# Optimization experiments

Hardware: AMD Instinct MI355X
Metric: run time of the kernel (lower is better)

Reference implementation:

```python
import jax, jax.numpy as jnp
import numpy as np

RF = 16       # receptive_field
STRIDE = 16   # sim_strides
ALPHA = 0.3   # tf.keras LeakyReLU default alpha
EPS = 1e-3    # tf.keras BatchNormalization default epsilon


def _leaky(x):
    return jnp.where(x > 0, x, ALPHA * x)


def _bn_train(x, gamma, beta):
    # training-mode batch norm over (B, H, W), channel-last
    mu = jnp.mean(x, axis=(0, 1, 2))
    var = jnp.var(x, axis=(0, 1, 2))
    return (x - mu) * jax.lax.rsqrt(var + EPS) * gamma + beta


def _cbl(x, W, gamma, beta):
    # 1x1 conv (== channel matmul) + BN + LeakyReLU
    y = jnp.einsum('bhwc,cd->bhwd', x, W)
    return _leaky(_bn_train(y, gamma, beta))


def setup_inputs() -> dict:
    key = jax.random.key(0)
    ks = jax.random.split(key, 4)
    B, H, Wd, C = 4, 64, 64, 256
    s = 1.0 / np.sqrt(C)
    return {
        'inputs': jax.random.normal(ks[0], (B, H, Wd, C), jnp.float32),
        'Wq': jax.random.normal(ks[1], (C, C), jnp.float32) * s,
        'gq': jnp.ones((C,), jnp.float32), 'bq': jnp.zeros((C,), jnp.float32),
        'Wk': jax.random.normal(ks[2], (C, C), jnp.float32) * s,
        'gk': jnp.ones((C,), jnp.float32), 'bk': jnp.zeros((C,), jnp.float32),
        'Wv': jax.random.normal(ks[3], (C, C), jnp.float32) * s,
        'gv': jnp.ones((C,), jnp.float32), 'bv': jnp.zeros((C,), jnp.float32),
        'g1': jnp.ones((C,), jnp.float32), 'b1': jnp.zeros((C,), jnp.float32),
    }


def _windows(x):
    # x: [B,H,W,C] -> [B, nH*nW, RF, RF, C] overlapping-capable window gather
    H, Wd = x.shape[1], x.shape[2]
    nH = (H - RF) // STRIDE + 1
    nW = (Wd - RF) // STRIDE + 1
    ih = (jnp.arange(nH) * STRIDE)[:, None] + jnp.arange(RF)[None, :]  # [nH,RF]
    iw = (jnp.arange(nW) * STRIDE)[:, None] + jnp.arange(RF)[None, :]  # [nW,RF]
    xw = x[:, ih][:, :, :, iw]            # [B,nH,RF,nW,RF,C]
    xw = xw.transpose(0, 1, 3, 2, 4, 5)   # [B,nH,nW,RF,RF,C]
    return xw.reshape(x.shape[0], nH * nW, RF, RF, x.shape[3])


def reference(inputs, Wq, gq, bq, Wk, gk, bk, Wv, gv, bv, g1, b1):
    Q = _cbl(inputs, Wq, gq, bq)   # [B,H,W,C]
    K = _cbl(inputs, Wk, gk, bk)
    V = _cbl(inputs, Wv, gv, bv)
    C = Q.shape[-1]
    Kw = _windows(K)               # [B,N,RF,RF,C]
    Vw = _windows(V)
    # full-Q x window-K attention, summed over windows (matches nested loop)
    scores = jnp.einsum('bijc,bnpqc->bnijpq', Q, Kw) / jnp.sqrt(jnp.asarray(C, Q.dtype))
    scores = _leaky(scores)
    yout = jnp.einsum('bnijpq,bnpqc->bijc', scores, Vw)  # sum over windows n
    y = _bn_train(yout, g1, b1)
    # softmax jointly over spatial axes (1,2)
    m = jnp.max(y, axis=(1, 2), keepdims=True)
    e = jnp.exp(y - m)
    return e / jnp.sum(e, axis=(1, 2), keepdims=True)
```

## Files before the change

kernel.cpp:

```cpp
#include <hip/hip_runtime.h>
#include <stdint.h>


typedef __attribute__((ext_vector_type(8)))  short short8;
typedef __attribute__((ext_vector_type(4)))  float f32x4;
typedef __attribute__((ext_vector_type(16))) float f32x16;
typedef __attribute__((ext_vector_type(4)))  unsigned short ushort4v;

#define ALPHA 0.3f
#define EPS   1e-3
#define NTOT  16384.0

__device__ __forceinline__ unsigned short f2bf(float f){
  unsigned u = __float_as_uint(f);
  u += 0x7FFFu + ((u>>16)&1u);
  return (unsigned short)(u>>16);
}
__device__ __forceinline__ float lrelu(float x){ return fmaxf(x, ALPHA*x); }

__global__ __launch_bounds__(256)
void k_prep(const float* __restrict__ X,
            const float* __restrict__ Wq,
            const float* __restrict__ Wk,
            const float* __restrict__ Wv,
            unsigned short* __restrict__ Xb,
            unsigned short* __restrict__ Wt,
            float* __restrict__ zws){
  int blk = blockIdx.x, tid = threadIdx.x;
  if (blk < 4096){
    int i = (blk*256 + tid)*4;
    float4 v = *(const float4*)(X + i);
    ushort4v o; o.x = f2bf(v.x); o.y = f2bf(v.y); o.z = f2bf(v.z); o.w = f2bf(v.w);
    *(ushort4v*)(Xb + i) = o;
  } else {
    int o = (blk - 4096)*256 + tid;
    int p = o >> 16, rem = o & 65535;
    int j = rem >> 8, c = rem & 255;
    const float* W = (p==0) ? Wq : ((p==1) ? Wk : Wv);
    Wt[o] = f2bf(W[c*256 + j]);
    if (o < 5120) zws[o] = 0.f;
  }
}

__global__ __launch_bounds__(256)
void k_qkv_gemm(const unsigned short* __restrict__ X,
                const unsigned short* __restrict__ Wt,
                float* __restrict__ YQK, float* __restrict__ Yv,
                double* __restrict__ st){
  __shared__ __align__(16) unsigned short At[64*264];
  __shared__ __align__(16) unsigned short Bt[64*264];
  int tid = threadIdx.x;
  int mb = blockIdx.x, nb = blockIdx.y;
#pragma unroll
  for (int it = 0; it < 8; ++it){
    int s = it*256 + tid;
    int row = s >> 5, ch = s & 31;
    uint4 a = *(const uint4*)(X  + ((size_t)(mb*64 + row))*256 + ch*8);
    uint4 b = *(const uint4*)(Wt + ((size_t)(nb*64 + row))*256 + ch*8);
    *(uint4*)(At + row*264 + ch*8) = a;
    *(uint4*)(Bt + row*264 + ch*8) = b;
  }
  __syncthreads();
  int lane = tid & 63, wv = tid >> 6;
  int ln15 = lane & 15, quad = lane >> 4;
  int rw = (wv & 1)*32, cw = (wv >> 1)*32;
  f32x4 acc[2][2] = {};
#pragma unroll
  for (int ks = 0; ks < 8; ++ks){
    short8 afr[2], bfr[2];
#pragma unroll
    for (int mt = 0; mt < 2; ++mt){
      int r = rw + mt*16 + ln15;
      afr[mt] = *(const short8*)(At + r*264 + (ks*4+quad)*8);
    }
#pragma unroll
    for (int nt = 0; nt < 2; ++nt){
      int r = cw + nt*16 + ln15;
      bfr[nt] = *(const short8*)(Bt + r*264 + (ks*4+quad)*8);
    }
#pragma unroll
    for (int mt = 0; mt < 2; ++mt)
#pragma unroll
      for (int nt = 0; nt < 2; ++nt)
        acc[mt][nt] = __builtin_amdgcn_mfma_f32_16x16x32_bf16(afr[mt], bfr[nt], acc[mt][nt], 0,0,0);
  }
  float ps[2] = {0.f, 0.f}, pq[2] = {0.f, 0.f};
#pragma unroll
  for (int mt = 0; mt < 2; ++mt)
#pragma unroll
    for (int nt = 0; nt < 2; ++nt)
#pragma unroll
      for (int r = 0; r < 4; ++r){
        float v = acc[mt][nt][r];
        ps[nt] += v; pq[nt] += v*v;
      }
  if (nb < 8){
    int proj = nb >> 2;
    float* base = YQK + (size_t)proj*(16384*256);
    int l5c = ln15 >> 3, j = ln15 & 7;
#pragma unroll
    for (int mt = 0; mt < 2; ++mt){
      int g = (mb*64 + rw + mt*16) >> 5;
      int l31r0 = ((rw + mt*16) & 31) + quad*4;
#pragma unroll
      for (int nt = 0; nt < 2; ++nt){
        int ks2 = ((nb & 3)*64 + cw + nt*16) >> 4;
#pragma unroll
        for (int r = 0; r < 4; ++r){
          size_t chunk = (size_t)((g*16 + ks2)*64 + l5c*32 + l31r0 + r);
          base[chunk*8 + j] = acc[mt][nt][r];
        }
      }
    }
  } else {
    int vc0 = (nb - 8)*64 + cw;
#pragma unroll
    for (int mt = 0; mt < 2; ++mt)
#pragma unroll
      for (int nt = 0; nt < 2; ++nt)
#pragma unroll
        for (int r = 0; r < 4; ++r){
          int row = mb*64 + rw + mt*16 + quad*4 + r;
          Yv[(size_t)row*256 + vc0 + nt*16 + ln15] = acc[mt][nt][r];
        }
  }
  __syncthreads();
  float* red = (float*)At;
  if (tid < 128) red[tid] = 0.f;
  __syncthreads();
#pragma unroll
  for (int nt = 0; nt < 2; ++nt){
    int colL = cw + nt*16 + ln15;
    atomicAdd(&red[colL],      ps[nt]);
    atomicAdd(&red[64 + colL], pq[nt]);
  }
  __syncthreads();
  if (tid < 64){
    int cc = nb*64 + tid;
    atomicAdd(&st[cc],       (double)red[tid]);
    atomicAdd(&st[768 + cc], (double)red[64 + tid]);
  }
}

__global__ __launch_bounds__(256)
void k_bn(const float* __restrict__ YQK, const float* __restrict__ Yv,
          const double* __restrict__ st,
          const float* __restrict__ gq, const float* __restrict__ bq,
          const float* __restrict__ gk, const float* __restrict__ bk,
          const float* __restrict__ gv, const float* __restrict__ bv,
          unsigned short* __restrict__ Qf, unsigned short* __restrict__ Kf,
          unsigned short* __restrict__ Vf){
  __shared__ float sc_s[256], sh_s[256];
  __shared__ unsigned short tile[64][66];
  int tid = threadIdx.x;
  int blk = blockIdx.x;
  if (blk < 4096){
    int proj = blk >> 11;
    {
      int c = tid;
      int cc = proj*256 + c;
      double mu  = st[cc]     * (1.0/NTOT);
      double var = st[768+cc] * (1.0/NTOT) - mu*mu;
      double g = proj ? (double)gk[c] : (double)gq[c];
      double b = proj ? (double)bk[c] : (double)bq[c];
      double a = g / sqrt(var + EPS);
      float f = proj ? 1.f : 0.0625f;
      sc_s[c] = (float)a * f;
      sh_s[c] = (float)(b - mu*a) * f;
    }
    __syncthreads();
    int oc = blk*256 + tid;
    int rest = oc & 524287;
    int ks = (rest >> 6) & 15, l5c = (rest >> 5) & 1;
    int ch0 = ks*16 + l5c*8;
    const float* src = YQK + (size_t)oc*8;
    float4 v0 = *(const float4*)(src);
    float4 v1 = *(const float4*)(src + 4);
    const float* sc = sc_s + ch0;
    const float* sh = sh_s + ch0;
    unsigned short r[8];
    r[0]=f2bf(lrelu(v0.x*sc[0]+sh[0])); r[1]=f2bf(lrelu(v0.y*sc[1]+sh[1]));
    r[2]=f2bf(lrelu(v0.z*sc[2]+sh[2])); r[3]=f2bf(lrelu(v0.w*sc[3]+sh[3]));
    r[4]=f2bf(lrelu(v1.x*sc[4]+sh[4])); r[5]=f2bf(lrelu(v1.y*sc[5]+sh[5]));
    r[6]=f2bf(lrelu(v1.z*sc[6]+sh[6])); r[7]=f2bf(lrelu(v1.w*sc[7]+sh[7]));
    uint4 u;
    u.x = (unsigned)r[0] | ((unsigned)r[1]<<16);
    u.y = (unsigned)r[2] | ((unsigned)r[3]<<16);
    u.z = (unsigned)r[4] | ((unsigned)r[5]<<16);
    u.w = (unsigned)r[6] | ((unsigned)r[7]<<16);
    *(uint4*)((proj ? Kf : Qf) + (size_t)rest*8) = u;
  } else {
    int b2 = blk - 4096;
    int pt = b2 & 63, ct = (b2 >> 6) & 3, b = b2 >> 8;
    if (tid < 64){
      int c = ct*64 + tid;
      int cc = 512 + c;
      double mu  = st[cc]     * (1.0/NTOT);
      double var = st[768+cc] * (1.0/NTOT) - mu*mu;
      double a = (double)gv[c] / sqrt(var + EPS);
      sc_s[tid] = (float)a;
      sh_s[tid] = (float)((double)bv[c] - mu*a);
    }
    __syncthreads();
    int cl = tid & 63, rq = tid >> 6;
    int c  = ct*64 + cl;
    float sc = sc_s[cl], sh = sh_s[cl];
#pragma unroll 4
    for (int k = 0; k < 16; ++k){
      int r = k*4 + rq;
      size_t t = (size_t)b*4096 + pt*64 + r;
      float v = Yv[t*256 + c];
      tile[r][cl] = f2bf(lrelu(v*sc + sh));
    }
    __syncthreads();
#pragma unroll
    for (int it = 0; it < 2; ++it){
      int m = it*256 + tid;
      int c2 = m >> 3, kg = m & 7;
      int ch = ct*64 + c2;
      int gc = b*8 + (ch >> 5), l31c = ch & 31;
      int kp = pt*4 + (kg >> 1), l5k = kg & 1;
      unsigned short r0 = tile[kg*8+0][c2], r1 = tile[kg*8+1][c2];
      unsigned short r2 = tile[kg*8+2][c2], r3 = tile[kg*8+3][c2];
      unsigned short r4 = tile[kg*8+4][c2], r5 = tile[kg*8+5][c2];
      unsigned short r6 = tile[kg*8+6][c2], r7 = tile[kg*8+7][c2];
      uint4 u;
      u.x = (unsigned)r0 | ((unsigned)r1<<16);
      u.y = (unsigned)r2 | ((unsigned)r3<<16);
      u.z = (unsigned)r4 | ((unsigned)r5<<16);
      u.w = (unsigned)r6 | ((unsigned)r7<<16);
      *(uint4*)(Vf + ((size_t)((gc*256 + kp)*64 + l5k*32 + l31c))*8) = u;
    }
  }
}

__global__ __launch_bounds__(512, 4)
void k_attn(const unsigned short* __restrict__ Qf,
            const unsigned short* __restrict__ Kf,
            const unsigned short* __restrict__ Vf,
            float* __restrict__ P0, float* __restrict__ P1){
  __shared__ __align__(16) unsigned short Ql[64*256];
  __shared__ __align__(16) unsigned short Sl[64*264];
  int tid = threadIdx.x;
  int blk = blockIdx.x;
  int qt = blk >> 3, combo = blk & 7;
  int b = combo >> 1, half = combo & 1;
  int q0 = qt*64;
  int lane = tid & 63, w = tid >> 6;
  int l31 = lane & 31, l5 = lane >> 5;
  float* P = half ? P1 : P0;

  int gq0 = b*128 + qt*2;
  {
    const uint4* src = (const uint4*)(Qf + (size_t)gq0*8192);
    uint4* dst = (uint4*)Ql;
#pragma unroll
    for (int it = 0; it < 4; ++it) dst[it*512 + tid] = src[it*512 + tid];
  }
  __syncthreads();

  f32x16 acc2[2] = {};
  int gk0 = b*128 + half*64 + w;
  const unsigned short* kb = Kf + (size_t)gk0*8192 + lane*8;
  const unsigned short* vb = Vf + ((size_t)((b*8 + w)*256 + half*128))*512 + lane*8;
  const unsigned short* qa0 = Ql + lane*8;
  const unsigned short* qa1 = Ql + 16*512 + lane*8;

  for (int kt = 0; kt < 8; ++kt){
    f32x16 a1[2] = {};
    const unsigned short* kbt = kb + (size_t)kt*8*8192;
    __builtin_amdgcn_s_setprio(1);
#pragma unroll
    for (int ks = 0; ks < 16; ++ks){
      short8 kf = *(const short8*)(kbt + ks*512);
      short8 q0v = *(const short8*)(qa0 + ks*512);
      short8 q1v = *(const short8*)(qa1 + ks*512);
      a1[0] = __builtin_amdgcn_mfma_f32_32x32x16_bf16(q0v, kf, a1[0], 0, 0, 0);
      a1[1] = __builtin_amdgcn_mfma_f32_32x32x16_bf16(q1v, kf, a1[1], 0, 0, 0);
    }
    __builtin_amdgcn_s_setprio(0);
    __syncthreads();
#pragma unroll
    for (int reg = 0; reg < 16; ++reg){
      int rloc = (reg & 3) + 8*(reg >> 2) + 4*l5;
      float x0 = a1[0][reg], x1 = a1[1][reg];
      Sl[rloc*264 + w*32 + l31]        = f2bf(fmaxf(x0, 0.3f*x0));
      Sl[(32 + rloc)*264 + w*32 + l31] = f2bf(fmaxf(x1, 0.3f*x1));
    }
    __syncthreads();
    const unsigned short* vbt = vb + (size_t)kt*16*512;
    __builtin_amdgcn_s_setprio(1);
#pragma unroll
    for (int kk = 0; kk < 16; ++kk){
      short8 vf = *(const short8*)(vbt + kk*512);
      short8 s0 = *(const short8*)(Sl + (     l31)*264 + kk*16 + l5*8);
      short8 s1 = *(const short8*)(Sl + (32 + l31)*264 + kk*16 + l5*8);
      acc2[0] = __builtin_amdgcn_mfma_f32_32x32x16_bf16(s0, vf, acc2[0], 0, 0, 0);
      acc2[1] = __builtin_amdgcn_mfma_f32_32x32x16_bf16(s1, vf, acc2[1], 0, 0, 0);
    }
    __builtin_amdgcn_s_setprio(0);
  }
#pragma unroll
  for (int c = 0; c < 2; ++c)
#pragma unroll
    for (int reg = 0; reg < 16; ++reg){
      int row = q0 + c*32 + (reg & 3) + 8*(reg >> 2) + 4*l5;
      P[((size_t)b*4096 + row)*256 + w*32 + l31] = acc2[c][reg];
    }
}

__global__ __launch_bounds__(256)
void k_red(const float* __restrict__ P0, const float* __restrict__ P1,
           float* __restrict__ yout, double* __restrict__ st){
  int tid = threadIdx.x;
  int r0 = blockIdx.x*32;
  double sum = 0, sq = 0;
#pragma unroll 4
  for (int r = 0; r < 32; ++r){
    size_t idx = (size_t)(r0 + r)*256 + tid;
    float v = P0[idx] + P1[idx];
    yout[idx] = v;
    sum += v; sq += (double)v*v;
  }
  atomicAdd(&st[1536 + tid], sum);
  atomicAdd(&st[1792 + tid], sq);
}

__global__ __launch_bounds__(256)
void k_soft1(const float* __restrict__ yout, const double* __restrict__ st,
             const float* __restrict__ g1, float* __restrict__ sums){
  __shared__ float red[256];
  __shared__ float sA[64], sK[64];
  int tid = threadIdx.x;
  int chunk = blockIdx.x, ct = blockIdx.y, b = blockIdx.z;
  int cl = tid & 63, pg = tid >> 6;
  int c = ct*64 + cl;
  if (tid < 64){
    int cc = ct*64 + tid;
    double mu  = st[1536 + cc]*(1.0/NTOT);
    double var = st[1792 + cc]*(1.0/NTOT) - mu*mu;
    double a = g1[cc] / sqrt(var + EPS);
    sA[tid] = (float)a;
    sK[tid] = (float)(a*mu);
  }
  __syncthreads();
  float a = sA[cl], K = sK[cl];
  float s = 0.f;
  const float* base = yout + ((size_t)b*4096 + chunk*256)*256 + c;
#pragma unroll 4
  for (int k = 0; k < 64; ++k){
    float v = base[(size_t)(pg + k*4)*256];
    s += __expf(v*a - K);
  }
  red[tid] = s;
  __syncthreads();
  if (tid < 64){
    float tot = red[tid] + red[64+tid] + red[128+tid] + red[192+tid];
    atomicAdd(&sums[b*256 + ct*64 + tid], tot);
  }
}

__global__ __launch_bounds__(256)
void k_soft2(const float* __restrict__ yout, const double* __restrict__ st,
             const float* __restrict__ g1, const float* __restrict__ sums,
             float* __restrict__ out){
  __shared__ float sA[64], sK[64], sR[64];
  int tid = threadIdx.x;
  int chunk = blockIdx.x, ct = blockIdx.y, b = blockIdx.z;
  int cl = tid & 63, pg = tid >> 6;
  int c = ct*64 + cl;
  if (tid < 64){
    int cc = ct*64 + tid;
    double mu  = st[1536 + cc]*(1.0/NTOT);
    double var = st[1792 + cc]*(1.0/NTOT) - mu*mu;
    double a = g1[cc] / sqrt(var + EPS);
    sA[tid] = (float)a;
    sK[tid] = (float)(a*mu);
    sR[tid] = 1.f / sums[b*256 + cc];
  }
  __syncthreads();
  float a = sA[cl], K = sK[cl], rl = sR[cl];
  const float* base = yout + ((size_t)b*4096 + chunk*256)*256 + c;
  float* obase = out + ((size_t)b*4096 + chunk*256)*256 + c;
#pragma unroll 4
  for (int k = 0; k < 64; ++k){
    size_t idx = (size_t)(pg + k*4)*256;
    obase[idx] = __expf(base[idx]*a - K) * rl;
  }
}

extern "C" void kernel_launch(void* const* d_in, const int* in_sizes, int n_in,
                              void* d_out, int out_size, void* d_ws, size_t ws_size,
                              hipStream_t stream){
  (void)in_sizes; (void)n_in; (void)out_size; (void)ws_size;
  const float* X  = (const float*)d_in[0];
  const float* Wq = (const float*)d_in[1];
  const float* gq = (const float*)d_in[2];
  const float* bq = (const float*)d_in[3];
  const float* Wk = (const float*)d_in[4];
  const float* gk = (const float*)d_in[5];
  const float* bk = (const float*)d_in[6];
  const float* Wv = (const float*)d_in[7];
  const float* gv = (const float*)d_in[8];
  const float* bv = (const float*)d_in[9];
  const float* g1 = (const float*)d_in[10];

  char* ws = (char*)d_ws;
  double*         st   = (double*)ws;
  float*          sums = (float*)(ws + 16384);
  unsigned short* Wt   = (unsigned short*)(ws + 26624);
  unsigned short* Xb   = (unsigned short*)(ws + 419840);
  float*          YQK  = (float*)(ws + 8808448);
  float*          Yv   = (float*)(ws + 42362880);
  unsigned short* Kf   = (unsigned short*)(ws + 59140096);
  unsigned short* Vf   = (unsigned short*)(ws + 67528704);
  unsigned short* Qf   = Xb;
  float*          P0   = YQK;
  float*          P1   = (float*)((char*)YQK + 16777216);
  float*          yo   = Yv;

  k_prep    <<<4864, 256, 0, stream>>>(X, Wq, Wk, Wv, Xb, Wt, (float*)st);
  k_qkv_gemm<<<dim3(256,12), 256, 0, stream>>>(Xb, Wt, YQK, Yv, st);
  k_bn      <<<5120, 256, 0, stream>>>(YQK, Yv, st, gq, bq, gk, bk, gv, bv, Qf, Kf, Vf);
  k_attn    <<<512, 512, 0, stream>>>(Qf, Kf, Vf, P0, P1);
  k_red     <<<512, 256, 0, stream>>>(P0, P1, yo, st);
  k_soft1   <<<dim3(16,4,4), 256, 0, stream>>>(yo, st, g1, sums);
  k_soft2   <<<dim3(16,4,4), 256, 0, stream>>>(yo, st, g1, sums, (float*)d_out);
}
```

Measured before the change: 251.2 us.

## Derive QKV batch-norm stats from input Gram matrix and fuse BN into GEMM

Instead of writing fp32 Q/K/V projections to memory, reducing their statistics, and running a separate BN pass, the code computes the input Gram matrix X^T X and per-channel input sums. From these it derives each projection channel's mean and variance as w^T G w and w·xsum. The QKV GEMM then applies BN scale/shift and LeakyReLU in its epilogue and writes bf16 in the attention layout directly. This removes large fp32 intermediate traffic and a kernel, but adds a Gram kernel with float atomics. It also computes variance as E[y²]−mu² in float from bf16 inputs, which may lose accuracy.

Measured after the change: 273.1 us. 1.09x slower.

```diff
diff --git a/kernel.cpp b/kernel.cpp
--- a/kernel.cpp
+++ b/kernel.cpp
@@ -16,7 +16,9 @@
   u += 0x7FFFu + ((u>>16)&1u);
   return (unsigned short)(u>>16);
 }
-__device__ __forceinline__ float lrelu(float x){ return fmaxf(x, ALPHA*x); }
+__device__ __forceinline__ float bf2f(unsigned short u){
+  return __uint_as_float((unsigned)u << 16);
+}
 
 __global__ __launch_bounds__(256)
 void k_prep(const float* __restrict__ X,
@@ -25,7 +27,7 @@
             const float* __restrict__ Wv,
             unsigned short* __restrict__ Xb,
             unsigned short* __restrict__ Wt,
-            float* __restrict__ zws){
+            float* __restrict__ Gz, float* __restrict__ stz){
   int blk = blockIdx.x, tid = threadIdx.x;
   if (blk < 4096){
     int i = (blk*256 + tid)*4;
@@ -33,24 +35,142 @@
     ushort4v o; o.x = f2bf(v.x); o.y = f2bf(v.y); o.z = f2bf(v.z); o.w = f2bf(v.w);
     *(ushort4v*)(Xb + i) = o;
   } else {
-    int o = (blk - 4096)*256 + tid;
+    int zb = blk - 4096;
+    int o = zb*256 + tid;
     int p = o >> 16, rem = o & 65535;
     int j = rem >> 8, c = rem & 255;
     const float* W = (p==0) ? Wq : ((p==1) ? Wk : Wv);
     Wt[o] = f2bf(W[c*256 + j]);
-    if (o < 5120) zws[o] = 0.f;
+    if (zb < 257)            Gz[o] = 0.f;
+    else if (zb < 265)       stz[(zb-257)*256 + tid] = 0.f;
+  }
+}
+
+__global__ __launch_bounds__(256)
+void k_gram(const unsigned short* __restrict__ Xb,
+            float* __restrict__ G, float* __restrict__ xsum){
+  __shared__ __align__(16) unsigned short At[64*72];
+  __shared__ __align__(16) unsigned short Bt[64*72];
+  int tid = threadIdx.x;
+  int ci = blockIdx.x, cj = blockIdx.y, ks = blockIdx.z;
+  bool diag = (ci == cj);
+  int lane = tid & 63, wv = tid >> 6;
+  int ln15 = lane & 15, quad = lane >> 4;
+  int rw = (wv & 1)*32, cw = (wv >> 1)*32;
+  f32x4 acc[2][2] = {};
+  float xs = 0.f;
+  int r0 = ks*1024;
+  int trl = tid >> 3, c8 = tid & 7;
+  for (int s = 0; s < 16; ++s){
+    int rbase = r0 + s*64;
+#pragma unroll
+    for (int i2 = 0; i2 < 2; ++i2){
+      int t = i2*32 + trl;
+      uint4 a = *(const uint4*)(Xb + ((size_t)(rbase + t))*256 + ci*64 + c8*8);
+      const unsigned short* ap = (const unsigned short*)&a;
+#pragma unroll
+      for (int e = 0; e < 8; ++e) At[(c8*8+e)*72 + t] = ap[e];
+      if (!diag){
+        uint4 b = *(const uint4*)(Xb + ((size_t)(rbase + t))*256 + cj*64 + c8*8);
+        const unsigned short* bp = (const unsigned short*)&b;
+#pragma unroll
+        for (int e = 0; e < 8; ++e) Bt[(c8*8+e)*72 + t] = bp[e];
+      }
+    }
+    __syncthreads();
+    if (diag && tid < 64){
+      float s2 = 0.f;
+      for (int t = 0; t < 64; ++t) s2 += bf2f(At[tid*72 + t]);
+      xs += s2;
+    }
+    const unsigned short* Bu = diag ? At : Bt;
+#pragma unroll
+    for (int k0 = 0; k0 < 2; ++k0){
+      short8 af[2], bf[2];
+#pragma unroll
+      for (int mt = 0; mt < 2; ++mt)
+        af[mt] = *(const short8*)(At + (rw+mt*16+ln15)*72 + k0*32 + quad*8);
+#pragma unroll
+      for (int nt = 0; nt < 2; ++nt)
+        bf[nt] = *(const short8*)(Bu + (cw+nt*16+ln15)*72 + k0*32 + quad*8);
+#pragma unroll
+      for (int mt = 0; mt < 2; ++mt)
+#pragma unroll
+        for (int nt = 0; nt < 2; ++nt)
+          acc[mt][nt] = __builtin_amdgcn_mfma_f32_16x16x32_bf16(af[mt], bf[nt], acc[mt][nt], 0,0,0);
+    }
+    __syncthreads();
+  }
+#pragma unroll
+  for (int mt = 0; mt < 2; ++mt)
+#pragma unroll
+    for (int nt = 0; nt < 2; ++nt)
+#pragma unroll
+      for (int r = 0; r < 4; ++r){
+        int gr = ci*64 + rw + mt*16 + quad*4 + r;
+        int gc = cj*64 + cw + nt*16 + ln15;
+        atomicAdd(&G[gr*256 + gc], acc[mt][nt][r]);
+      }
+  if (diag && tid < 64) atomicAdd(&xsum[ci*64 + tid], xs);
+}
+
+__global__ __launch_bounds__(256)
+void k_coef2(const float* __restrict__ G, const float* __restrict__ xsum,
+             const unsigned short* __restrict__ Wt,
+             const float* __restrict__ gq, const float* __restrict__ bq,
+             const float* __restrict__ gk, const float* __restrict__ bk,
+             const float* __restrict__ gv, const float* __restrict__ bv,
+             float* __restrict__ scv, float* __restrict__ shv){
+  __shared__ float wv_s[256];
+  __shared__ float red1[256], red2[256];
+  int n = blockIdx.x;
+  int c = threadIdx.x;
+  float w = bf2f(Wt[n*256 + c]);
+  wv_s[c] = w;
+  __syncthreads();
+  const float* gr = G + c*256;
+  float dot = 0.f;
+#pragma unroll 8
+  for (int c2 = 0; c2 < 256; c2 += 4){
+    float4 g4 = *(const float4*)(gr + c2);
+    dot += g4.x*wv_s[c2] + g4.y*wv_s[c2+1] + g4.z*wv_s[c2+2] + g4.w*wv_s[c2+3];
+  }
+  red1[c] = w * dot;
+  red2[c] = xsum[c] * w;
+  __syncthreads();
+  for (int off = 128; off > 0; off >>= 1){
+    if (c < off){ red1[c] += red1[c+off]; red2[c] += red2[c+off]; }
+    __syncthreads();
+  }
+  if (c == 0){
+    double ms = (double)red1[0] * (1.0/NTOT);
+    double mu = (double)red2[0] * (1.0/NTOT);
+    double var = ms - mu*mu;
+    int proj = n >> 8, ch = n & 255;
+    double g = (proj==0) ? gq[ch] : (proj==1) ? gk[ch] : gv[ch];
+    double b = (proj==0) ? bq[ch] : (proj==1) ? bk[ch] : bv[ch];
+    double a = g / sqrt(var + EPS);
+    double f = (proj==0) ? 0.0625 : 1.0;
+    scv[n] = (float)(a*f);
+    shv[n] = (float)((b - mu*a)*f);
   }
 }
 
 __global__ __launch_bounds__(256)
 void k_qkv_gemm(const unsigned short* __restrict__ X,
                 const unsigned short* __restrict__ Wt,
-                float* __restrict__ YQK, float* __restrict__ Yv,
-                double* __restrict__ st){
+                const float* __restrict__ scv, const float* __restrict__ shv,
+                unsigned short* __restrict__ Qf, unsigned short* __restrict__ Kf,
+                unsigned short* __restrict__ Vf){
   __shared__ __align__(16) unsigned short At[64*264];
   __shared__ __align__(16) unsigned short Bt[64*264];
+  __shared__ float cf_sc[64], cf_sh[64];
   int tid = threadIdx.x;
   int mb = blockIdx.x, nb = blockIdx.y;
+  if (tid < 64){
+    int idx = (nb < 8) ? ((nb>>2)*256 + (nb&3)*64 + tid) : (512 + (nb-8)*64 + tid);
+    cf_sc[tid] = scv[idx]; cf_sh[tid] = shv[idx];
+  }
 #pragma unroll
   for (int it = 0; it < 8; ++it){
     int s = it*256 + tid;
@@ -84,151 +204,57 @@
       for (int nt = 0; nt < 2; ++nt)
         acc[mt][nt] = __builtin_amdgcn_mfma_f32_16x16x32_bf16(afr[mt], bfr[nt], acc[mt][nt], 0,0,0);
   }
-  float ps[2] = {0.f, 0.f}, pq[2] = {0.f, 0.f};
+  float scr[2], shr[2];
+#pragma unroll
+  for (int nt = 0; nt < 2; ++nt){
+    int cl = cw + nt*16 + ln15;
+    scr[nt] = cf_sc[cl]; shr[nt] = cf_sh[cl];
+  }
+  __syncthreads();
+  unsigned short* tile = (unsigned short*)At;
 #pragma unroll
   for (int mt = 0; mt < 2; ++mt)
 #pragma unroll
     for (int nt = 0; nt < 2; ++nt)
 #pragma unroll
       for (int r = 0; r < 4; ++r){
-        float v = acc[mt][nt][r];
-        ps[nt] += v; pq[nt] += v*v;
+        int row = rw + mt*16 + quad*4 + r;
+        int col = cw + nt*16 + ln15;
+        float v = acc[mt][nt][r]*scr[nt] + shr[nt];
+        tile[row*72 + col] = f2bf(fmaxf(v, ALPHA*v));
       }
+  __syncthreads();
   if (nb < 8){
-    int proj = nb >> 2;
-    float* base = YQK + (size_t)proj*(16384*256);
-    int l5c = ln15 >> 3, j = ln15 & 7;
-#pragma unroll
-    for (int mt = 0; mt < 2; ++mt){
-      int g = (mb*64 + rw + mt*16) >> 5;
-      int l31r0 = ((rw + mt*16) & 31) + quad*4;
-#pragma unroll
-      for (int nt = 0; nt < 2; ++nt){
-        int ks2 = ((nb & 3)*64 + cw + nt*16) >> 4;
-#pragma unroll
-        for (int r = 0; r < 4; ++r){
-          size_t chunk = (size_t)((g*16 + ks2)*64 + l5c*32 + l31r0 + r);
-          base[chunk*8 + j] = acc[mt][nt][r];
-        }
-      }
-    }
-  } else {
-    int vc0 = (nb - 8)*64 + cw;
-#pragma unroll
-    for (int mt = 0; mt < 2; ++mt)
-#pragma unroll
-      for (int nt = 0; nt < 2; ++nt)
-#pragma unroll
-        for (int r = 0; r < 4; ++r){
-          int row = mb*64 + rw + mt*16 + quad*4 + r;
-          Yv[(size_t)row*256 + vc0 + nt*16 + ln15] = acc[mt][nt][r];
-        }
-  }
-  __syncthreads();
-  float* red = (float*)At;
-  if (tid < 128) red[tid] = 0.f;
-  __syncthreads();
-#pragma unroll
-  for (int nt = 0; nt < 2; ++nt){
-    int colL = cw + nt*16 + ln15;
-    atomicAdd(&red[colL],      ps[nt]);
-    atomicAdd(&red[64 + colL], pq[nt]);
-  }
-  __syncthreads();
-  if (tid < 64){
-    int cc = nb*64 + tid;
-    atomicAdd(&st[cc],       (double)red[tid]);
-    atomicAdd(&st[768 + cc], (double)red[64 + tid]);
-  }
-}
-
-__global__ __launch_bounds__(256)
-void k_bn(const float* __restrict__ YQK, const float* __restrict__ Yv,
-          const double* __restrict__ st,
-          const float* __restrict__ gq, const float* __restrict__ bq,
-          const float* __restrict__ gk, const float* __restrict__ bk,
-          const float* __restrict__ gv, const float* __restrict__ bv,
-          unsigned short* __restrict__ Qf, unsigned short* __restrict__ Kf,
-          unsigned short* __restrict__ Vf){
-  __shared__ float sc_s[256], sh_s[256];
-  __shared__ unsigned short tile[64][66];
-  int tid = threadIdx.x;
-  int blk = blockIdx.x;
-  if (blk < 4096){
-    int proj = blk >> 11;
-    {
-      int c = tid;
-      int cc = proj*256 + c;
-      double mu  = st[cc]     * (1.0/NTOT);
-      double var = st[768+cc] * (1.0/NTOT) - mu*mu;
-      double g = proj ? (double)gk[c] : (double)gq[c];
-      double b = proj ? (double)bk[c] : (double)bq[c];
-      double a = g / sqrt(var + EPS);
-      float f = proj ? 1.f : 0.0625f;
-      sc_s[c] = (float)a * f;
-      sh_s[c] = (float)(b - mu*a) * f;
-    }
-    __syncthreads();
-    int oc = blk*256 + tid;
-    int rest = oc & 524287;
-    int ks = (rest >> 6) & 15, l5c = (rest >> 5) & 1;
-    int ch0 = ks*16 + l5c*8;
-    const float* src = YQK + (size_t)oc*8;
-    float4 v0 = *(const float4*)(src);
-    float4 v1 = *(const float4*)(src + 4);
-    const float* sc = sc_s + ch0;
-    const float* sh = sh_s + ch0;
-    unsigned short r[8];
-    r[0]=f2bf(lrelu(v0.x*sc[0]+sh[0])); r[1]=f2bf(lrelu(v0.y*sc[1]+sh[1]));
-    r[2]=f2bf(lrelu(v0.z*sc[2]+sh[2])); r[3]=f2bf(lrelu(v0.w*sc[3]+sh[3]));
-    r[4]=f2bf(lrelu(v1.x*sc[4]+sh[4])); r[5]=f2bf(lrelu(v1.y*sc[5]+sh[5]));
-    r[6]=f2bf(lrelu(v1.z*sc[6]+sh[6])); r[7]=f2bf(lrelu(v1.w*sc[7]+sh[7]));
-    uint4 u;
-    u.x = (unsigned)r[0] | ((unsigned)r[1]<<16);
-    u.y = (unsigned)r[2] | ((unsigned)r[3]<<16);
-    u.z = (unsigned)r[4] | ((unsigned)r[5]<<16);
-    u.w = (unsigned)r[6] | ((unsigned)r[7]<<16);
-    *(uint4*)((proj ? Kf : Qf) + (size_t)rest*8) = u;
-  } else {
-    int b2 = blk - 4096;
-    int pt = b2 & 63, ct = (b2 >> 6) & 3, b = b2 >> 8;
-    if (tid < 64){
-      int c = ct*64 + tid;
-      int cc = 512 + c;
-      double mu  = st[cc]     * (1.0/NTOT);
-      double var = st[768+cc] * (1.0/NTOT) - mu*mu;
-      double a = (double)gv[c] / sqrt(var + EPS);
-      sc_s[tid] = (float)a;
-      sh_s[tid] = (float)((double)bv[c] - mu*a);
-    }
-    __syncthreads();
-    int cl = tid & 63, rq = tid >> 6;
-    int c  = ct*64 + cl;
-    float sc = sc_s[cl], sh = sh_s[cl];
-#pragma unroll 4
-    for (int k = 0; k < 16; ++k){
-      int r = k*4 + rq;
-      size_t t = (size_t)b*4096 + pt*64 + r;
-      float v = Yv[t*256 + c];
-      tile[r][cl] = f2bf(lrelu(v*sc + sh));
-    }
-    __syncthreads();
+    unsigned short* dstB = (nb >> 2) ? Kf : Qf;
 #pragma unroll
     for (int it = 0; it < 2; ++it){
       int m = it*256 + tid;
-      int c2 = m >> 3, kg = m & 7;
-      int ch = ct*64 + c2;
-      int gc = b*8 + (ch >> 5), l31c = ch & 31;
-      int kp = pt*4 + (kg >> 1), l5k = kg & 1;
-      unsigned short r0 = tile[kg*8+0][c2], r1 = tile[kg*8+1][c2];
-      unsigned short r2 = tile[kg*8+2][c2], r3 = tile[kg*8+3][c2];
-      unsigned short r4 = tile[kg*8+4][c2], r5 = tile[kg*8+5][c2];
-      unsigned short r6 = tile[kg*8+6][c2], r7 = tile[kg*8+7][c2];
+      int cg = m >> 6, row = m & 63;
+      uint4 u = *(const uint4*)(tile + row*72 + cg*8);
+      int ch_g = (nb&3)*64 + cg*8;
+      int ksf = ch_g >> 4, l5c = (ch_g >> 3) & 1;
+      int row_g = mb*64 + row;
+      int g = row_g >> 5, l31r = row_g & 31;
+      *(uint4*)(dstB + ((size_t)((g*16 + ksf)*64 + l5c*32 + l31r))*8) = u;
+    }
+  } else {
+    int b = mb >> 6;
+#pragma unroll
+    for (int it = 0; it < 2; ++it){
+      int m = it*256 + tid;
+      int chl = m & 63, pg = m >> 6;
+      unsigned short r0 = tile[(pg*8+0)*72 + chl], r1 = tile[(pg*8+1)*72 + chl];
+      unsigned short r2 = tile[(pg*8+2)*72 + chl], r3 = tile[(pg*8+3)*72 + chl];
+      unsigned short r4 = tile[(pg*8+4)*72 + chl], r5 = tile[(pg*8+5)*72 + chl];
+      unsigned short r6 = tile[(pg*8+6)*72 + chl], r7 = tile[(pg*8+7)*72 + chl];
       uint4 u;
       u.x = (unsigned)r0 | ((unsigned)r1<<16);
       u.y = (unsigned)r2 | ((unsigned)r3<<16);
       u.z = (unsigned)r4 | ((unsigned)r5<<16);
       u.w = (unsigned)r6 | ((unsigned)r7<<16);
+      int ch_g = (nb-8)*64 + chl;
+      int gc = b*8 + (ch_g >> 5), l31c = ch_g & 31;
+      int kp = (mb&63)*4 + (pg >> 1), l5k = pg & 1;
       *(uint4*)(Vf + ((size_t)((gc*256 + kp)*64 + l5k*32 + l31c))*8) = u;
     }
   }
@@ -310,7 +336,7 @@
 }
 
 __global__ __launch_bounds__(256)
-void k_red(const float* __restrict__ P0, const float* __restrict__ P1,
+void k_red(const float* __restrict__ P0c, const float* __restrict__ P1,
            float* __restrict__ yout, double* __restrict__ st){
   int tid = threadIdx.x;
   int r0 = blockIdx.x*32;
@@ -318,7 +344,7 @@
 #pragma unroll 4
   for (int r = 0; r < 32; ++r){
     size_t idx = (size_t)(r0 + r)*256 + tid;
-    float v = P0[idx] + P1[idx];
+    float v = P0c[idx] + P1[idx];
     yout[idx] = v;
     sum += v; sq += (double)v*v;
   }
@@ -407,21 +433,25 @@
 
   char* ws = (char*)d_ws;
   double*         st   = (double*)ws;
+  float*          stz  = (float*)(ws + 12288);
   float*          sums = (float*)(ws + 16384);
+  float*          scv  = (float*)(ws + 20480);
+  float*          shv  = (float*)(ws + 23552);
   unsigned short* Wt   = (unsigned short*)(ws + 26624);
   unsigned short* Xb   = (unsigned short*)(ws + 419840);
-  float*          YQK  = (float*)(ws + 8808448);
-  float*          Yv   = (float*)(ws + 42362880);
-  unsigned short* Kf   = (unsigned short*)(ws + 59140096);
-  unsigned short* Vf   = (unsigned short*)(ws + 67528704);
-  unsigned short* Qf   = Xb;
-  float*          P0   = YQK;
-  float*          P1   = (float*)((char*)YQK + 16777216);
-  float*          yo   = Yv;
-
-  k_prep    <<<4864, 256, 0, stream>>>(X, Wq, Wk, Wv, Xb, Wt, (float*)st);
-  k_qkv_gemm<<<dim3(256,12), 256, 0, stream>>>(Xb, Wt, YQK, Yv, st);
-  k_bn      <<<5120, 256, 0, stream>>>(YQK, Yv, st, gq, bq, gk, bk, gv, bv, Qf, Kf, Vf);
+  float*          G    = (float*)(ws + 8808448);
+  float*          xsum = (float*)(ws + 9070592);
+  unsigned short* Qf   = (unsigned short*)(ws + 17301504);
+  unsigned short* Kf   = (unsigned short*)(ws + 25690112);
+  unsigned short* Vf   = (unsigned short*)(ws + 34078720);
+  float*          P0   = (float*)(ws + 419840);
+  float*          P1   = (float*)(ws + 42467328);
+  float*          yo   = P0;
+
+  k_prep    <<<4864, 256, 0, stream>>>(X, Wq, Wk, Wv, Xb, Wt, G, stz);
+  k_gram    <<<dim3(4,4,16), 256, 0, stream>>>(Xb, G, xsum);
+  k_coef2   <<<768, 256, 0, stream>>>(G, xsum, Wt, gq, bq, gk, bk, gv, bv, scv, shv);
+  k_qkv_gemm<<<dim3(256,12), 256, 0, stream>>>(Xb, Wt, scv, shv, Qf, Kf, Vf);
   k_attn    <<<512, 512, 0, stream>>>(Qf, Kf, Vf, P0, P1);
   k_red     <<<512, 256, 0, stream>>>(P0, P1, yo, st);
   k_soft1   <<<dim3(16,4,4), 256, 0, stream>>>(yo, st, g1, sums);
```

## Fuse split-K reduction into attention epilogue and merge softmax passes cooperatively

Applied to the files above, without the earlier changes.

The attention kernel now has the second-finishing block of each half pair, detected with an atomic counter, add the partner's partial sum, write the combined result and accumulate the batch-norm statistics. This removes the separate reduction kernel and one full read/write pass over the partials. The two softmax kernels become one cooperative kernel that keeps the exponentials in registers across a grid-wide sync, so the activations are read once instead of twice. In exchange it adds a threadfence/atomic handshake, a large per-thread register array, and a dependency on cooperative launch residency.

Measured after the change: 458.8 us. 82.6% more time.

```diff
diff --git a/kernel.cpp b/kernel.cpp
--- a/kernel.cpp
+++ b/kernel.cpp
@@ -1,5 +1,8 @@
 #include <hip/hip_runtime.h>
+#include <hip/hip_cooperative_groups.h>
 #include <stdint.h>
+
+namespace cg = cooperative_groups;
 
 
 typedef __attribute__((ext_vector_type(8)))  short short8;
@@ -38,7 +41,7 @@
     int j = rem >> 8, c = rem & 255;
     const float* W = (p==0) ? Wq : ((p==1) ? Wk : Wv);
     Wt[o] = f2bf(W[c*256 + j]);
-    if (o < 5120) zws[o] = 0.f;
+    if (o < 5376) zws[o] = 0.f;
   }
 }
 
@@ -238,7 +241,8 @@
 void k_attn(const unsigned short* __restrict__ Qf,
             const unsigned short* __restrict__ Kf,
             const unsigned short* __restrict__ Vf,
-            float* __restrict__ P0, float* __restrict__ P1){
+            float* __restrict__ P0, float* __restrict__ P1,
+            unsigned* __restrict__ cnt, double* __restrict__ st){
   __shared__ __align__(16) unsigned short Ql[64*256];
   __shared__ __align__(16) unsigned short Sl[64*264];
   int tid = threadIdx.x;
@@ -307,63 +311,40 @@
       int row = q0 + c*32 + (reg & 3) + 8*(reg >> 2) + 4*l5;
       P[((size_t)b*4096 + row)*256 + w*32 + l31] = acc2[c][reg];
     }
+  __threadfence();
+  __shared__ unsigned sOld;
+  __syncthreads();
+  if (tid == 0) sOld = atomicAdd(&cnt[(b<<6) + qt], 1u);
+  __syncthreads();
+  if (sOld == 0) return;
+  __threadfence();
+  const float* Po = half ? P0 : P1;
+  double sum = 0.0, sq = 0.0;
+#pragma unroll
+  for (int c = 0; c < 2; ++c)
+#pragma unroll
+    for (int reg = 0; reg < 16; ++reg){
+      int row = q0 + c*32 + (reg & 3) + 8*(reg >> 2) + 4*l5;
+      size_t idx = ((size_t)b*4096 + row)*256 + w*32 + l31;
+      float v = acc2[c][reg] + Po[idx];
+      P0[idx] = v;
+      sum += v; sq += (double)v*v;
+    }
+  double* redS = (double*)Sl;
+  redS[tid] = sum; redS[512 + tid] = sq;
+  __syncthreads();
+  if ((tid & 32) == 0){
+    int c = ((tid >> 6) << 5) + (tid & 31);
+    atomicAdd(&st[1536 + c], redS[tid] + redS[tid + 32]);
+    atomicAdd(&st[1792 + c], redS[512 + tid] + redS[512 + tid + 32]);
+  }
 }
 
 __global__ __launch_bounds__(256)
-void k_red(const float* __restrict__ P0, const float* __restrict__ P1,
-           float* __restrict__ yout, double* __restrict__ st){
-  int tid = threadIdx.x;
-  int r0 = blockIdx.x*32;
-  double sum = 0, sq = 0;
-#pragma unroll 4
-  for (int r = 0; r < 32; ++r){
-    size_t idx = (size_t)(r0 + r)*256 + tid;
-    float v = P0[idx] + P1[idx];
-    yout[idx] = v;
-    sum += v; sq += (double)v*v;
-  }
-  atomicAdd(&st[1536 + tid], sum);
-  atomicAdd(&st[1792 + tid], sq);
-}
-
-__global__ __launch_bounds__(256)
-void k_soft1(const float* __restrict__ yout, const double* __restrict__ st,
-             const float* __restrict__ g1, float* __restrict__ sums){
+void k_soft(const float* __restrict__ yout, const double* __restrict__ st,
+            const float* __restrict__ g1, float* __restrict__ sums,
+            float* __restrict__ out){
   __shared__ float red[256];
-  __shared__ float sA[64], sK[64];
-  int tid = threadIdx.x;
-  int chunk = blockIdx.x, ct = blockIdx.y, b = blockIdx.z;
-  int cl = tid & 63, pg = tid >> 6;
-  int c = ct*64 + cl;
-  if (tid < 64){
-    int cc = ct*64 + tid;
-    double mu  = st[1536 + cc]*(1.0/NTOT);
-    double var = st[1792 + cc]*(1.0/NTOT) - mu*mu;
-    double a = g1[cc] / sqrt(var + EPS);
-    sA[tid] = (float)a;
-    sK[tid] = (float)(a*mu);
-  }
-  __syncthreads();
-  float a = sA[cl], K = sK[cl];
-  float s = 0.f;
-  const float* base = yout + ((size_t)b*4096 + chunk*256)*256 + c;
-#pragma unroll 4
-  for (int k = 0; k < 64; ++k){
-    float v = base[(size_t)(pg + k*4)*256];
-    s += __expf(v*a - K);
-  }
-  red[tid] = s;
-  __syncthreads();
-  if (tid < 64){
-    float tot = red[tid] + red[64+tid] + red[128+tid] + red[192+tid];
-    atomicAdd(&sums[b*256 + ct*64 + tid], tot);
-  }
-}
-
-__global__ __launch_bounds__(256)
-void k_soft2(const float* __restrict__ yout, const double* __restrict__ st,
-             const float* __restrict__ g1, const float* __restrict__ sums,
-             float* __restrict__ out){
   __shared__ float sA[64], sK[64], sR[64];
   int tid = threadIdx.x;
   int chunk = blockIdx.x, ct = blockIdx.y, b = blockIdx.z;
@@ -376,17 +357,32 @@
     double a = g1[cc] / sqrt(var + EPS);
     sA[tid] = (float)a;
     sK[tid] = (float)(a*mu);
-    sR[tid] = 1.f / sums[b*256 + cc];
-  }
-  __syncthreads();
-  float a = sA[cl], K = sK[cl], rl = sR[cl];
+  }
+  __syncthreads();
+  float a = sA[cl], K = sK[cl];
+  float e[64];
+  float s = 0.f;
   const float* base = yout + ((size_t)b*4096 + chunk*256)*256 + c;
+#pragma unroll
+  for (int k = 0; k < 64; ++k){
+    float v = base[(size_t)(pg + k*4)*256];
+    e[k] = __expf(v*a - K);
+    s += e[k];
+  }
+  red[tid] = s;
+  __syncthreads();
+  if (tid < 64){
+    float tot = red[tid] + red[64+tid] + red[128+tid] + red[192+tid];
+    atomicAdd(&sums[b*256 + ct*64 + tid], tot);
+  }
+  cg::this_grid().sync();
+  if (tid < 64) sR[tid] = 1.f / sums[b*256 + ct*64 + tid];
+  __syncthreads();
+  float rl = sR[cl];
   float* obase = out + ((size_t)b*4096 + chunk*256)*256 + c;
-#pragma unroll 4
-  for (int k = 0; k < 64; ++k){
-    size_t idx = (size_t)(pg + k*4)*256;
-    obase[idx] = __expf(base[idx]*a - K) * rl;
-  }
+#pragma unroll
+  for (int k = 0; k < 64; ++k)
+    obase[(size_t)(pg + k*4)*256] = e[k] * rl;
 }
 
 extern "C" void kernel_launch(void* const* d_in, const int* in_sizes, int n_in,
@@ -408,6 +404,7 @@
   char* ws = (char*)d_ws;
   double*         st   = (double*)ws;
   float*          sums = (float*)(ws + 16384);
+  unsigned*       cnt  = (unsigned*)(ws + 20480);
   unsigned short* Wt   = (unsigned short*)(ws + 26624);
   unsigned short* Xb   = (unsigned short*)(ws + 419840);
   float*          YQK  = (float*)(ws + 8808448);
@@ -417,13 +414,21 @@
   unsigned short* Qf   = Xb;
   float*          P0   = YQK;
   float*          P1   = (float*)((char*)YQK + 16777216);
-  float*          yo   = Yv;
+  float*          yo   = P0;
+  float*          outp = (float*)d_out;
 
   k_prep    <<<4864, 256, 0, stream>>>(X, Wq, Wk, Wv, Xb, Wt, (float*)st);
   k_qkv_gemm<<<dim3(256,12), 256, 0, stream>>>(Xb, Wt, YQK, Yv, st);
   k_bn      <<<5120, 256, 0, stream>>>(YQK, Yv, st, gq, bq, gk, bk, gv, bv, Qf, Kf, Vf);
-  k_attn    <<<512, 512, 0, stream>>>(Qf, Kf, Vf, P0, P1);
-  k_red     <<<512, 256, 0, stream>>>(P0, P1, yo, st);
-  k_soft1   <<<dim3(16,4,4), 256, 0, stream>>>(yo, st, g1, sums);
-  k_soft2   <<<dim3(16,4,4), 256, 0, stream>>>(yo, st, g1, sums, (float*)d_out);
-}
+  k_attn    <<<512, 512, 0, stream>>>(Qf, Kf, Vf, P0, P1, cnt, st);
+  {
+    void* sargs[5];
+    sargs[0] = (void*)&yo;
+    sargs[1] = (void*)&st;
+    sargs[2] = (void*)&g1;
+    sargs[3] = (void*)&sums;
+    sargs[4] = (void*)&outp;
+    hipLaunchCooperativeKernel((const void*)k_soft, dim3(16,4,4), dim3(256,1,1),
+                               sargs, 0, stream);
+  }
+}
```

## Fuse reduction, BN stats and softmax into one cooperative kernel with grid syncs

Applied to the files above, without the earlier changes.

Replaces the three tail kernels (partial reduce, softmax sum, softmax write) with a single cooperative kernel. Each thread keeps its 32 reduced values in registers and uses two grid-wide syncs: one to wait for the BN statistics, one for the softmax denominators. This removes the round trips of yout through global memory and two kernel launches. In exchange it depends on all 512 blocks being co-resident and pays for two grid barriers.

Result: slower. 356.8 us (+42.0%).

```diff
diff --git a/kernel.cpp b/kernel.cpp
--- a/kernel.cpp
+++ b/kernel.cpp
@@ -1,5 +1,8 @@
 #include <hip/hip_runtime.h>
+#include <hip/hip_cooperative_groups.h>
 #include <stdint.h>
+
+namespace cg = cooperative_groups;
 
 
 typedef __attribute__((ext_vector_type(8)))  short short8;
@@ -310,82 +313,42 @@
 }
 
 __global__ __launch_bounds__(256)
-void k_red(const float* __restrict__ P0, const float* __restrict__ P1,
-           float* __restrict__ yout, double* __restrict__ st){
+void k_rs(const float* __restrict__ P0, const float* __restrict__ P1,
+          double* __restrict__ st, const float* __restrict__ g1,
+          float* __restrict__ sums, float* __restrict__ out){
   int tid = threadIdx.x;
-  int r0 = blockIdx.x*32;
-  double sum = 0, sq = 0;
-#pragma unroll 4
+  int blk = blockIdx.x;
+  int r0 = blk*32;
+  int b = blk >> 7;
+  float e[32];
+  double sum = 0.0, sq = 0.0;
+#pragma unroll
   for (int r = 0; r < 32; ++r){
     size_t idx = (size_t)(r0 + r)*256 + tid;
     float v = P0[idx] + P1[idx];
-    yout[idx] = v;
+    e[r] = v;
     sum += v; sq += (double)v*v;
   }
   atomicAdd(&st[1536 + tid], sum);
   atomicAdd(&st[1792 + tid], sq);
-}
-
-__global__ __launch_bounds__(256)
-void k_soft1(const float* __restrict__ yout, const double* __restrict__ st,
-             const float* __restrict__ g1, float* __restrict__ sums){
-  __shared__ float red[256];
-  __shared__ float sA[64], sK[64];
-  int tid = threadIdx.x;
-  int chunk = blockIdx.x, ct = blockIdx.y, b = blockIdx.z;
-  int cl = tid & 63, pg = tid >> 6;
-  int c = ct*64 + cl;
-  if (tid < 64){
-    int cc = ct*64 + tid;
-    double mu  = st[1536 + cc]*(1.0/NTOT);
-    double var = st[1792 + cc]*(1.0/NTOT) - mu*mu;
-    double a = g1[cc] / sqrt(var + EPS);
-    sA[tid] = (float)a;
-    sK[tid] = (float)(a*mu);
-  }
-  __syncthreads();
-  float a = sA[cl], K = sK[cl];
+  cg::this_grid().sync();
+  double mu  = st[1536 + tid]*(1.0/NTOT);
+  double var = st[1792 + tid]*(1.0/NTOT) - mu*mu;
+  double ad  = (double)g1[tid] / sqrt(var + EPS);
+  float a = (float)ad, K = (float)(ad*mu);
   float s = 0.f;
-  const float* base = yout + ((size_t)b*4096 + chunk*256)*256 + c;
-#pragma unroll 4
-  for (int k = 0; k < 64; ++k){
-    float v = base[(size_t)(pg + k*4)*256];
-    s += __expf(v*a - K);
-  }
-  red[tid] = s;
-  __syncthreads();
-  if (tid < 64){
-    float tot = red[tid] + red[64+tid] + red[128+tid] + red[192+tid];
-    atomicAdd(&sums[b*256 + ct*64 + tid], tot);
-  }
-}
-
-__global__ __launch_bounds__(256)
-void k_soft2(const float* __restrict__ yout, const double* __restrict__ st,
-             const float* __restrict__ g1, const float* __restrict__ sums,
-             float* __restrict__ out){
-  __shared__ float sA[64], sK[64], sR[64];
-  int tid = threadIdx.x;
-  int chunk = blockIdx.x, ct = blockIdx.y, b = blockIdx.z;
-  int cl = tid & 63, pg = tid >> 6;
-  int c = ct*64 + cl;
-  if (tid < 64){
-    int cc = ct*64 + tid;
-    double mu  = st[1536 + cc]*(1.0/NTOT);
-    double var = st[1792 + cc]*(1.0/NTOT) - mu*mu;
-    double a = g1[cc] / sqrt(var + EPS);
-    sA[tid] = (float)a;
-    sK[tid] = (float)(a*mu);
-    sR[tid] = 1.f / sums[b*256 + cc];
-  }
-  __syncthreads();
-  float a = sA[cl], K = sK[cl], rl = sR[cl];
-  const float* base = yout + ((size_t)b*4096 + chunk*256)*256 + c;
-  float* obase = out + ((size_t)b*4096 + chunk*256)*256 + c;
-#pragma unroll 4
-  for (int k = 0; k < 64; ++k){
-    size_t idx = (size_t)(pg + k*4)*256;
-    obase[idx] = __expf(base[idx]*a - K) * rl;
+#pragma unroll
+  for (int r = 0; r < 32; ++r){
+    e[r] = __expf(e[r]*a - K);
+    s += e[r];
+  }
+  atomicAdd(&sums[b*256 + tid], s);
+  cg::this_grid().sync();
+  float rl = 1.f / sums[b*256 + tid];
+#pragma unroll
+  for (int r = 0; r < 32; ++r){
+    size_t idx = (size_t)(r0 + r)*256 + tid;
+    out[idx] = e[r]*rl;
   }
 }
 
@@ -417,13 +380,21 @@
   unsigned short* Qf   = Xb;
   float*          P0   = YQK;
   float*          P1   = (float*)((char*)YQK + 16777216);
-  float*          yo   = Yv;
+  float*          outp = (float*)d_out;
 
   k_prep    <<<4864, 256, 0, stream>>>(X, Wq, Wk, Wv, Xb, Wt, (float*)st);
   k_qkv_gemm<<<dim3(256,12), 256, 0, stream>>>(Xb, Wt, YQK, Yv, st);
   k_bn      <<<5120, 256, 0, stream>>>(YQK, Yv, st, gq, bq, gk, bk, gv, bv, Qf, Kf, Vf);
   k_attn    <<<512, 512, 0, stream>>>(Qf, Kf, Vf, P0, P1);
-  k_red     <<<512, 256, 0, stream>>>(P0, P1, yo, st);
-  k_soft1   <<<dim3(16,4,4), 256, 0, stream>>>(yo, st, g1, sums);
-  k_soft2   <<<dim3(16,4,4), 256, 0, stream>>>(yo, st, g1, sums, (float*)d_out);
-}
+  {
+    void* sargs[6];
+    sargs[0] = (void*)&P0;
+    sargs[1] = (void*)&P1;
+    sargs[2] = (void*)&st;
+    sargs[3] = (void*)&g1;
+    sargs[4] = (void*)&sums;
+    sargs[5] = (void*)&outp;
+    hipLaunchCooperativeKernel((const void*)k_rs, dim3(512,1,1), dim3(256,1,1),
+                               sargs, 0, stream);
+  }
+}
```
